# Optimization experiments

Measured on AMD Instinct MI355X. Metric: run time of the kernel, lower is better.

The kernel has to match this reference:

```python
import jax, jax.numpy as jnp
import numpy as np


def setup_inputs() -> dict:
    key = jax.random.key(0)
    k1, k2, k3, k4, k5 = jax.random.split(key, 5)
    B, T, D, H = 128, 512, 128, 512
    x = jax.random.normal(k1, (B, T, D), dtype=jnp.float32)
    h = jnp.zeros((B, H), dtype=jnp.float32)
    # tau in [1, 2) so the Euler step h + (-h + upd)/tau is stable
    tau = jax.random.uniform(k2, (B, 1), dtype=jnp.float32) + 1.0
    s_in = 1.0 / np.sqrt(D)
    s_rec = 1.0 / np.sqrt(H)
    # torch nn.Linear default init: U(-1/sqrt(fan_in), 1/sqrt(fan_in))
    W_in_w = jax.random.uniform(k3, (H, D), dtype=jnp.float32, minval=-s_in, maxval=s_in)
    W_in_b = jax.random.uniform(k4, (H,), dtype=jnp.float32, minval=-s_in, maxval=s_in)
    W_rec_w = jax.random.uniform(k5, (H, H), dtype=jnp.float32, minval=-s_rec, maxval=s_rec)
    return {"x": x, "h": h, "tau": tau, "W_in_w": W_in_w, "W_in_b": W_in_b, "W_rec_w": W_rec_w}


def reference(x, h, tau, W_in_w, W_in_b, W_rec_w):
    # Precompute the input projection for all timesteps in one big GEMM.
    # x: [B,T,D], W_in_w: [H,D] -> x_in: [B,T,H]
    x_in = jnp.einsum('btd,hd->bth', x, W_in_w) + W_in_b

    def step(h_t, xin_t):
        # xin_t: [B,H]; recurrent GEMM + tanh + Euler update (true data dep on h_t)
        upd = jnp.tanh(xin_t + h_t @ W_rec_w.T)
        h_new = h_t + (-h_t + upd) / tau
        return h_new, h_new

    h_last, h_seq = jax.lax.scan(step, h, jnp.swapaxes(x_in, 0, 1))  # scan over T
    return jnp.swapaxes(h_seq, 0, 1), h_last  # ([B,T,H], [B,H])
```

## Files before the change

### kernel.cpp

```cpp
#include <hip/hip_runtime.h>

#define B_SZ 128
#define T_SZ 512
#define D_SZ 128
#define H_SZ 512

#define NG 8
#define GB 16
#define NS 4
#define SN 128

typedef _Float16 f16;
typedef _Float16 f16x8 __attribute__((ext_vector_type(8)));
typedef _Float16 f16x4 __attribute__((ext_vector_type(4)));
typedef float f32x4 __attribute__((ext_vector_type(4)));
typedef unsigned long long ull;
typedef unsigned int uint;

__global__ __launch_bounds__(256) void input_proj_mfma(
    const float* __restrict__ x,
    const float* __restrict__ Win,
    const float* __restrict__ bias,
    float* __restrict__ out)
{
  const int tid = threadIdx.x;
  const int w = tid >> 6;
  const int l = tid & 63;
  const int m = l & 15;
  const int kg = l >> 4;
  const int ht = w * 128;

  f16x8 af[8][4];
#pragma unroll
  for (int t = 0; t < 8; ++t) {
    const float* wr = Win + (size_t)(ht + t * 16 + m) * D_SZ;
#pragma unroll
    for (int kb = 0; kb < 4; ++kb) {
      const int k0 = kb * 32 + kg * 8;
      float4 u0 = *(const float4*)(wr + k0);
      float4 u1 = *(const float4*)(wr + k0 + 4);
      f16x8 a;
      a[0] = (f16)u0.x; a[1] = (f16)u0.y; a[2] = (f16)u0.z; a[3] = (f16)u0.w;
      a[4] = (f16)u1.x; a[5] = (f16)u1.y; a[6] = (f16)u1.z; a[7] = (f16)u1.w;
      af[t][kb] = a;
    }
  }

  for (int rt = 0; rt < 8; ++rt) {
    const size_t r0 = ((size_t)blockIdx.x * 8 + rt) * 16;
    const float* xr = x + (r0 + m) * D_SZ + kg * 8;
    f16x8 bf[4];
#pragma unroll
    for (int kb = 0; kb < 4; ++kb) {
      float4 u0 = *(const float4*)(xr + kb * 32);
      float4 u1 = *(const float4*)(xr + kb * 32 + 4);
      f16x8 a;
      a[0] = (f16)u0.x; a[1] = (f16)u0.y; a[2] = (f16)u0.z; a[3] = (f16)u0.w;
      a[4] = (f16)u1.x; a[5] = (f16)u1.y; a[6] = (f16)u1.z; a[7] = (f16)u1.w;
      bf[kb] = a;
    }
    f32x4 acc[8];
#pragma unroll
    for (int t = 0; t < 8; ++t) acc[t] = (f32x4){0.f, 0.f, 0.f, 0.f};
#pragma unroll
    for (int kb = 0; kb < 4; ++kb)
#pragma unroll
      for (int t = 0; t < 8; ++t)
        acc[t] = __builtin_amdgcn_mfma_f32_16x16x32_f16(af[t][kb], bf[kb], acc[t], 0, 0, 0);
#pragma unroll
    for (int t = 0; t < 8; ++t) {
      const int c0 = ht + t * 16 + kg * 4;
      float4 bb = *(const float4*)(bias + c0);
      float4 o;
      o.x = acc[t][0] + bb.x;
      o.y = acc[t][1] + bb.y;
      o.z = acc[t][2] + bb.z;
      o.w = acc[t][3] + bb.w;
      *(float4*)(out + (r0 + m) * H_SZ + c0) = o;
    }
  }
}

__device__ __forceinline__ float fast_tanh(float y) {
  float e = __expf(2.0f * y);
  return 1.0f - __fdividef(2.0f, e + 1.0f);
}

__device__ __forceinline__ ull ld_agent(const ull* p) {
  return __hip_atomic_load(p, __ATOMIC_RELAXED, __HIP_MEMORY_SCOPE_AGENT);
}

__global__ __launch_bounds__(512) void ltc_rec_mfma(
    float* __restrict__ seq,
    float* __restrict__ h_last,
    const float* __restrict__ hin,
    const float* __restrict__ tau,
    const float* __restrict__ Wrec,
    f16* __restrict__ ex)
{
  __shared__ f16 hs[2][GB * H_SZ];

  const int tid = threadIdx.x;
  const int g = blockIdx.x & 7;
  const int slice = blockIdx.x >> 3;
  const int w = tid >> 6;
  const int l = tid & 63;
  const int m = l & 15;
  const int kg = l >> 4;
  const int jt = slice * SN + w * 16;
  const int j0 = jt + kg * 4;
  const int b = g * GB + m;

  f16x8 afrag[16];
  {
    const float* wr = Wrec + (size_t)(jt + m) * H_SZ;
#pragma unroll
    for (int ff = 0; ff < 16; ++ff) {
      const int f = (slice * 4 + ff) & 15;
      const int k0 = f * 32 + kg * 8;
      float4 u0 = *(const float4*)(wr + k0);
      float4 u1 = *(const float4*)(wr + k0 + 4);
      f16x8 a;
      a[0] = (f16)u0.x; a[1] = (f16)u0.y; a[2] = (f16)u0.z; a[3] = (f16)u0.w;
      a[4] = (f16)u1.x; a[5] = (f16)u1.y; a[6] = (f16)u1.z; a[7] = (f16)u1.w;
      afrag[ff] = a;
    }
  }

  float hreg[4];
  {
    float4 h0 = *(const float4*)(hin + (size_t)b * H_SZ + j0);
    hreg[0] = h0.x; hreg[1] = h0.y; hreg[2] = h0.z; hreg[3] = h0.w;
  }
  const float itau = 1.0f / tau[b];

  {
    const int mr = tid >> 5;
    const int c4 = (tid & 31) * 4;
#pragma unroll
    for (int p = 0; p < 4; ++p) {
      const int col = p * SN + c4;
      float4 v = *(const float4*)(hin + (size_t)(g * GB + mr) * H_SZ + col);
      const int e = (mr * H_SZ + col) ^ ((mr & 7) << 3);
      f16x4 hf;
      hf[0] = (f16)v.x; hf[1] = (f16)v.y; hf[2] = (f16)v.z; hf[3] = (f16)v.w;
      *(f16x4*)&hs[0][e] = hf;
    }
  }
  __syncthreads();

  const size_t EXB = (size_t)GB * SN;
  const size_t RING_ULL = (size_t)NG * NS * EXB / 4;
  ull* pub0 = (ull*)(ex + ((size_t)g * NS + slice) * EXB + (size_t)m * SN + (w * 16 + kg * 4));

  const int gmr = tid >> 5;
  const int gc4 = (tid & 31) * 4;
  const int psa = (slice + 1) & 3, psb = (slice + 2) & 3, psc = (slice + 3) & 3;
  const ull* ga0 = (const ull*)(ex + ((size_t)g * NS + psa) * EXB + (size_t)gmr * SN + gc4);
  const ull* gb0 = (const ull*)(ex + ((size_t)g * NS + psb) * EXB + (size_t)gmr * SN + gc4);
  const ull* gc0 = (const ull*)(ex + ((size_t)g * NS + psc) * EXB + (size_t)gmr * SN + gc4);
  const int ea = (gmr * H_SZ + psa * SN + gc4) ^ ((gmr & 7) << 3);
  const int eb = (gmr * H_SZ + psb * SN + gc4) ^ ((gmr & 7) << 3);
  const int ec = (gmr * H_SZ + psc * SN + gc4) ^ ((gmr & 7) << 3);
  const int eown = (m * H_SZ + j0) ^ ((m & 7) << 3);

  int ebase[16];
#pragma unroll
  for (int ff = 0; ff < 16; ++ff) {
    const int f = (slice * 4 + ff) & 15;
    ebase[ff] = (m * H_SZ + f * 32 + kg * 8) ^ ((m & 7) << 3);
  }

  float* seqp = seq + (size_t)b * T_SZ * H_SZ + j0;
  float4 xin = *(const float4*)seqp;

  for (int s = 0; s < T_SZ; ++s) {
    const int cur = s & 1, nxt = cur ^ 1;

    ull w0 = 0, w1 = 0, w2 = 0;
    const size_t proff = nxt ? RING_ULL : 0;
    const ull ptag = (ull)(((s - 1) >> 1) & 1);
    if (s > 0) {
      w0 = ld_agent(ga0 + proff);
      w1 = ld_agent(gb0 + proff);
      w2 = ld_agent(gc0 + proff);
    }

    f32x4 accA = {0.f, 0.f, 0.f, 0.f};
    accA = __builtin_amdgcn_mfma_f32_16x16x32_f16(afrag[0], *(const f16x8*)&hs[cur][ebase[0]], accA, 0, 0, 0);
    accA = __builtin_amdgcn_mfma_f32_16x16x32_f16(afrag[1], *(const f16x8*)&hs[cur][ebase[1]], accA, 0, 0, 0);
    accA = __builtin_amdgcn_mfma_f32_16x16x32_f16(afrag[2], *(const f16x8*)&hs[cur][ebase[2]], accA, 0, 0, 0);
    accA = __builtin_amdgcn_mfma_f32_16x16x32_f16(afrag[3], *(const f16x8*)&hs[cur][ebase[3]], accA, 0, 0, 0);

    if (s > 0) {
      while ((w0 & 1ULL) != ptag) w0 = ld_agent(ga0 + proff);
      while ((w1 & 1ULL) != ptag) w1 = ld_agent(gb0 + proff);
      while ((w2 & 1ULL) != ptag) w2 = ld_agent(gc0 + proff);
      *(f16x4*)&hs[cur][ea] = __builtin_bit_cast(f16x4, w0);
      *(f16x4*)&hs[cur][eb] = __builtin_bit_cast(f16x4, w1);
      *(f16x4*)&hs[cur][ec] = __builtin_bit_cast(f16x4, w2);
      __syncthreads();
    }

    f32x4 accB = {0.f, 0.f, 0.f, 0.f};
    f32x4 accC = {0.f, 0.f, 0.f, 0.f};
    accB = __builtin_amdgcn_mfma_f32_16x16x32_f16(afrag[4],  *(const f16x8*)&hs[cur][ebase[4]],  accB, 0, 0, 0);
    accB = __builtin_amdgcn_mfma_f32_16x16x32_f16(afrag[5],  *(const f16x8*)&hs[cur][ebase[5]],  accB, 0, 0, 0);
    accB = __builtin_amdgcn_mfma_f32_16x16x32_f16(afrag[6],  *(const f16x8*)&hs[cur][ebase[6]],  accB, 0, 0, 0);
    accB = __builtin_amdgcn_mfma_f32_16x16x32_f16(afrag[7],  *(const f16x8*)&hs[cur][ebase[7]],  accB, 0, 0, 0);
    accB = __builtin_amdgcn_mfma_f32_16x16x32_f16(afrag[8],  *(const f16x8*)&hs[cur][ebase[8]],  accB, 0, 0, 0);
    accB = __builtin_amdgcn_mfma_f32_16x16x32_f16(afrag[9],  *(const f16x8*)&hs[cur][ebase[9]],  accB, 0, 0, 0);
    accC = __builtin_amdgcn_mfma_f32_16x16x32_f16(afrag[10], *(const f16x8*)&hs[cur][ebase[10]], accC, 0, 0, 0);
    accC = __builtin_amdgcn_mfma_f32_16x16x32_f16(afrag[11], *(const f16x8*)&hs[cur][ebase[11]], accC, 0, 0, 0);
    accC = __builtin_amdgcn_mfma_f32_16x16x32_f16(afrag[12], *(const f16x8*)&hs[cur][ebase[12]], accC, 0, 0, 0);
    accC = __builtin_amdgcn_mfma_f32_16x16x32_f16(afrag[13], *(const f16x8*)&hs[cur][ebase[13]], accC, 0, 0, 0);
    accC = __builtin_amdgcn_mfma_f32_16x16x32_f16(afrag[14], *(const f16x8*)&hs[cur][ebase[14]], accC, 0, 0, 0);
    accC = __builtin_amdgcn_mfma_f32_16x16x32_f16(afrag[15], *(const f16x8*)&hs[cur][ebase[15]], accC, 0, 0, 0);
    f32x4 acc = accA + accB + accC;

    float4 hv;
    hv.x = fmaf(fast_tanh(xin.x + acc[0]) - hreg[0], itau, hreg[0]);
    hv.y = fmaf(fast_tanh(xin.y + acc[1]) - hreg[1], itau, hreg[1]);
    hv.z = fmaf(fast_tanh(xin.z + acc[2]) - hreg[2], itau, hreg[2]);
    hv.w = fmaf(fast_tanh(xin.w + acc[3]) - hreg[3], itau, hreg[3]);
    hreg[0] = hv.x; hreg[1] = hv.y; hreg[2] = hv.z; hreg[3] = hv.w;

    f16x4 hf;
    hf[0] = (f16)hv.x; hf[1] = (f16)hv.y; hf[2] = (f16)hv.z; hf[3] = (f16)hv.w;

    {
      ull bits = __builtin_bit_cast(ull, hf);
      bits = (bits & ~1ULL) | (ull)((s >> 1) & 1);
      __hip_atomic_store(pub0 + (cur ? RING_ULL : 0), bits,
                         __ATOMIC_RELAXED, __HIP_MEMORY_SCOPE_AGENT);
    }

    *(f16x4*)&hs[nxt][eown] = hf;
    *(float4*)seqp = hv;
    seqp += H_SZ;
    xin = *(const float4*)seqp;

    __syncthreads();
  }

  float4 hv;
  hv.x = hreg[0]; hv.y = hreg[1]; hv.z = hreg[2]; hv.w = hreg[3];
  *(float4*)(h_last + (size_t)b * H_SZ + j0) = hv;
}

extern "C" void kernel_launch(void* const* d_in, const int* in_sizes, int n_in,
                              void* d_out, int out_size, void* d_ws, size_t ws_size,
                              hipStream_t stream) {
  const float* x     = (const float*)d_in[0];
  const float* hin   = (const float*)d_in[1];
  const float* tau   = (const float*)d_in[2];
  const float* Win_w = (const float*)d_in[3];
  const float* Win_b = (const float*)d_in[4];
  const float* Wrec  = (const float*)d_in[5];

  float* out    = (float*)d_out;
  float* seq    = out;
  float* h_last = out + (size_t)B_SZ * T_SZ * H_SZ;

  f16* ex = (f16*)d_ws;

  hipMemsetAsync(ex, 0xFF, 2 * NG * NS * GB * SN * sizeof(f16), stream);

  input_proj_mfma<<<512, 256, 0, stream>>>(x, Win_w, Win_b, seq);
  ltc_rec_mfma<<<NG * NS, 512, 0, stream>>>(seq, h_last, hin, tau, Wrec, ex);
}
```

Measured before the change: 976.8 us.

## Split K across wave pairs and reduce partial sums through LDS

Each pair of waves now covers two 16-column output tiles, and each wave handles half of the K dimension (8 of 16 fragments). One B fragment load from LDS then feeds two MFMAs, which halves LDS reads per MFMA and shortens the dependent MFMA chain per wave. Partial sums are exchanged through a new LDS reduction buffer with an extra barrier each timestep, so the cost is one more block-wide sync on the serial recurrence path.

```diff
diff --git a/kernel.cpp b/kernel.cpp
--- a/kernel.cpp
+++ b/kernel.cpp
@@ -16,6 +16,14 @@
 typedef float f32x4 __attribute__((ext_vector_type(4)));
 typedef unsigned long long ull;
 typedef unsigned int uint;
+
+#define BAR_LGKM()                                         \
+  do {                                                     \
+    asm volatile("s_waitcnt lgkmcnt(0)" ::: "memory");     \
+    __builtin_amdgcn_sched_barrier(0);                     \
+    __builtin_amdgcn_s_barrier();                          \
+    __builtin_amdgcn_sched_barrier(0);                     \
+  } while (0)
 
 __global__ __launch_bounds__(256) void input_proj_mfma(
     const float* __restrict__ x,
@@ -99,31 +107,46 @@
     f16* __restrict__ ex)
 {
   __shared__ f16 hs[2][GB * H_SZ];
+  __shared__ __attribute__((aligned(16))) float red[8 * 64 * 4];
 
   const int tid = threadIdx.x;
   const int g = blockIdx.x & 7;
   const int slice = blockIdx.x >> 3;
   const int w = tid >> 6;
+  const int jg = w & 3;
+  const int kh = w >> 2;
   const int l = tid & 63;
   const int m = l & 15;
   const int kg = l >> 4;
-  const int jt = slice * SN + w * 16;
-  const int j0 = jt + kg * 4;
+  const int t0 = 2 * jg;
+  const int t_own = 2 * jg + kh;
+  const int j0 = slice * SN + t_own * 16 + kg * 4;
   const int b = g * GB + m;
-
-  f16x8 afrag[16];
+  const int msk = (m & 7) << 3;
+
+  f16x8 af0[8], af1[8];
+  int ebase[8];
   {
-    const float* wr = Wrec + (size_t)(jt + m) * H_SZ;
-#pragma unroll
-    for (int ff = 0; ff < 16; ++ff) {
-      const int f = (slice * 4 + ff) & 15;
+    const float* wrA = Wrec + (size_t)(slice * SN + t0 * 16 + m) * H_SZ;
+    const float* wrB = wrA + 16 * H_SZ;
+#pragma unroll
+    for (int i = 0; i < 8; ++i) {
+      const int f = (i < 2 ? (slice * 4 + 2 * kh + i)
+                           : (slice * 4 + 4 + 6 * kh + (i - 2))) & 15;
       const int k0 = f * 32 + kg * 8;
-      float4 u0 = *(const float4*)(wr + k0);
-      float4 u1 = *(const float4*)(wr + k0 + 4);
+      float4 u0 = *(const float4*)(wrA + k0);
+      float4 u1 = *(const float4*)(wrA + k0 + 4);
       f16x8 a;
       a[0] = (f16)u0.x; a[1] = (f16)u0.y; a[2] = (f16)u0.z; a[3] = (f16)u0.w;
       a[4] = (f16)u1.x; a[5] = (f16)u1.y; a[6] = (f16)u1.z; a[7] = (f16)u1.w;
-      afrag[ff] = a;
+      af0[i] = a;
+      float4 v0 = *(const float4*)(wrB + k0);
+      float4 v1 = *(const float4*)(wrB + k0 + 4);
+      f16x8 c;
+      c[0] = (f16)v0.x; c[1] = (f16)v0.y; c[2] = (f16)v0.z; c[3] = (f16)v0.w;
+      c[4] = (f16)v1.x; c[5] = (f16)v1.y; c[6] = (f16)v1.z; c[7] = (f16)v1.w;
+      af1[i] = c;
+      ebase[i] = (m * H_SZ + f * 32 + kg * 8) ^ msk;
     }
   }
 
@@ -151,7 +174,7 @@
 
   const size_t EXB = (size_t)GB * SN;
   const size_t RING_ULL = (size_t)NG * NS * EXB / 4;
-  ull* pub0 = (ull*)(ex + ((size_t)g * NS + slice) * EXB + (size_t)m * SN + (w * 16 + kg * 4));
+  ull* pub0 = (ull*)(ex + ((size_t)g * NS + slice) * EXB + (size_t)m * SN + (t_own * 16 + kg * 4));
 
   const int gmr = tid >> 5;
   const int gc4 = (tid & 31) * 4;
@@ -162,14 +185,10 @@
   const int ea = (gmr * H_SZ + psa * SN + gc4) ^ ((gmr & 7) << 3);
   const int eb = (gmr * H_SZ + psb * SN + gc4) ^ ((gmr & 7) << 3);
   const int ec = (gmr * H_SZ + psc * SN + gc4) ^ ((gmr & 7) << 3);
-  const int eown = (m * H_SZ + j0) ^ ((m & 7) << 3);
-
-  int ebase[16];
-#pragma unroll
-  for (int ff = 0; ff < 16; ++ff) {
-    const int f = (slice * 4 + ff) & 15;
-    ebase[ff] = (m * H_SZ + f * 32 + kg * 8) ^ ((m & 7) << 3);
-  }
+  const int eown = (m * H_SZ + j0) ^ msk;
+
+  float* redw = red + ((size_t)(jg * 2 + kh) * 64 + l) * 4;
+  const float* redr = red + ((size_t)(jg * 2 + (1 - kh)) * 64 + l) * 4;
 
   float* seqp = seq + (size_t)b * T_SZ * H_SZ + j0;
   float4 xin = *(const float4*)seqp;
@@ -186,11 +205,16 @@
       w2 = ld_agent(gc0 + proff);
     }
 
-    f32x4 accA = {0.f, 0.f, 0.f, 0.f};
-    accA = __builtin_amdgcn_mfma_f32_16x16x32_f16(afrag[0], *(const f16x8*)&hs[cur][ebase[0]], accA, 0, 0, 0);
-    accA = __builtin_amdgcn_mfma_f32_16x16x32_f16(afrag[1], *(const f16x8*)&hs[cur][ebase[1]], accA, 0, 0, 0);
-    accA = __builtin_amdgcn_mfma_f32_16x16x32_f16(afrag[2], *(const f16x8*)&hs[cur][ebase[2]], accA, 0, 0, 0);
-    accA = __builtin_amdgcn_mfma_f32_16x16x32_f16(afrag[3], *(const f16x8*)&hs[cur][ebase[3]], accA, 0, 0, 0);
+    f32x4 acc0 = {0.f, 0.f, 0.f, 0.f};
+    f32x4 acc1 = {0.f, 0.f, 0.f, 0.f};
+    {
+      f16x8 bf = *(const f16x8*)&hs[cur][ebase[0]];
+      acc0 = __builtin_amdgcn_mfma_f32_16x16x32_f16(af0[0], bf, acc0, 0, 0, 0);
+      acc1 = __builtin_amdgcn_mfma_f32_16x16x32_f16(af1[0], bf, acc1, 0, 0, 0);
+      bf = *(const f16x8*)&hs[cur][ebase[1]];
+      acc0 = __builtin_amdgcn_mfma_f32_16x16x32_f16(af0[1], bf, acc0, 0, 0, 0);
+      acc1 = __builtin_amdgcn_mfma_f32_16x16x32_f16(af1[1], bf, acc1, 0, 0, 0);
+    }
 
     if (s > 0) {
       while ((w0 & 1ULL) != ptag) w0 = ld_agent(ga0 + proff);
@@ -202,21 +226,33 @@
       __syncthreads();
     }
 
-    f32x4 accB = {0.f, 0.f, 0.f, 0.f};
-    f32x4 accC = {0.f, 0.f, 0.f, 0.f};
-    accB = __builtin_amdgcn_mfma_f32_16x16x32_f16(afrag[4],  *(const f16x8*)&hs[cur][ebase[4]],  accB, 0, 0, 0);
-    accB = __builtin_amdgcn_mfma_f32_16x16x32_f16(afrag[5],  *(const f16x8*)&hs[cur][ebase[5]],  accB, 0, 0, 0);
-    accB = __builtin_amdgcn_mfma_f32_16x16x32_f16(afrag[6],  *(const f16x8*)&hs[cur][ebase[6]],  accB, 0, 0, 0);
-    accB = __builtin_amdgcn_mfma_f32_16x16x32_f16(afrag[7],  *(const f16x8*)&hs[cur][ebase[7]],  accB, 0, 0, 0);
-    accB = __builtin_amdgcn_mfma_f32_16x16x32_f16(afrag[8],  *(const f16x8*)&hs[cur][ebase[8]],  accB, 0, 0, 0);
-    accB = __builtin_amdgcn_mfma_f32_16x16x32_f16(afrag[9],  *(const f16x8*)&hs[cur][ebase[9]],  accB, 0, 0, 0);
-    accC = __builtin_amdgcn_mfma_f32_16x16x32_f16(afrag[10], *(const f16x8*)&hs[cur][ebase[10]], accC, 0, 0, 0);
-    accC = __builtin_amdgcn_mfma_f32_16x16x32_f16(afrag[11], *(const f16x8*)&hs[cur][ebase[11]], accC, 0, 0, 0);
-    accC = __builtin_amdgcn_mfma_f32_16x16x32_f16(afrag[12], *(const f16x8*)&hs[cur][ebase[12]], accC, 0, 0, 0);
-    accC = __builtin_amdgcn_mfma_f32_16x16x32_f16(afrag[13], *(const f16x8*)&hs[cur][ebase[13]], accC, 0, 0, 0);
-    accC = __builtin_amdgcn_mfma_f32_16x16x32_f16(afrag[14], *(const f16x8*)&hs[cur][ebase[14]], accC, 0, 0, 0);
-    accC = __builtin_amdgcn_mfma_f32_16x16x32_f16(afrag[15], *(const f16x8*)&hs[cur][ebase[15]], accC, 0, 0, 0);
-    f32x4 acc = accA + accB + accC;
+    {
+      f16x8 bf = *(const f16x8*)&hs[cur][ebase[2]];
+      acc0 = __builtin_amdgcn_mfma_f32_16x16x32_f16(af0[2], bf, acc0, 0, 0, 0);
+      acc1 = __builtin_amdgcn_mfma_f32_16x16x32_f16(af1[2], bf, acc1, 0, 0, 0);
+      bf = *(const f16x8*)&hs[cur][ebase[3]];
+      acc0 = __builtin_amdgcn_mfma_f32_16x16x32_f16(af0[3], bf, acc0, 0, 0, 0);
+      acc1 = __builtin_amdgcn_mfma_f32_16x16x32_f16(af1[3], bf, acc1, 0, 0, 0);
+      bf = *(const f16x8*)&hs[cur][ebase[4]];
+      acc0 = __builtin_amdgcn_mfma_f32_16x16x32_f16(af0[4], bf, acc0, 0, 0, 0);
+      acc1 = __builtin_amdgcn_mfma_f32_16x16x32_f16(af1[4], bf, acc1, 0, 0, 0);
+      bf = *(const f16x8*)&hs[cur][ebase[5]];
+      acc0 = __builtin_amdgcn_mfma_f32_16x16x32_f16(af0[5], bf, acc0, 0, 0, 0);
+      acc1 = __builtin_amdgcn_mfma_f32_16x16x32_f16(af1[5], bf, acc1, 0, 0, 0);
+      bf = *(const f16x8*)&hs[cur][ebase[6]];
+      acc0 = __builtin_amdgcn_mfma_f32_16x16x32_f16(af0[6], bf, acc0, 0, 0, 0);
+      acc1 = __builtin_amdgcn_mfma_f32_16x16x32_f16(af1[6], bf, acc1, 0, 0, 0);
+      bf = *(const f16x8*)&hs[cur][ebase[7]];
+      acc0 = __builtin_amdgcn_mfma_f32_16x16x32_f16(af0[7], bf, acc0, 0, 0, 0);
+      acc1 = __builtin_amdgcn_mfma_f32_16x16x32_f16(af1[7], bf, acc1, 0, 0, 0);
+    }
+
+    f32x4 accOwnP, accOth;
+    if (kh == 0) { accOwnP = acc0; accOth = acc1; }
+    else         { accOwnP = acc1; accOth = acc0; }
+    *(f32x4*)redw = accOth;
+    BAR_LGKM();
+    f32x4 acc = accOwnP + *(const f32x4*)redr;
 
     float4 hv;
     hv.x = fmaf(fast_tanh(xin.x + acc[0]) - hreg[0], itau, hreg[0]);
```

After: 984.2 us. No clear change (+0.8%).
